# Kernel optimization log

Hardware: AMD Instinct MI355X
Metric: run time of the kernel (lower is better)

## Reference

```python
import jax, jax.numpy as jnp
import numpy as np

D_MODEL = 1024
HEADS = 16
HEAD_DIM = D_MODEL // HEADS


def setup_inputs() -> dict:
    key = jax.random.key(0)
    k_x, k_q, k_k, k_v, k_o = jax.random.split(key, 5)
    B, S = 4, 2048
    return {
        "x": jax.random.normal(k_x, (B, S, D_MODEL), dtype=jnp.float32),
        "W_q": jax.random.normal(k_q, (D_MODEL, D_MODEL), dtype=jnp.float32),
        "W_k": jax.random.normal(k_k, (D_MODEL, D_MODEL), dtype=jnp.float32),
        "W_v": jax.random.normal(k_v, (D_MODEL, D_MODEL), dtype=jnp.float32),
        "fc_out": jax.random.normal(k_o, (D_MODEL, D_MODEL), dtype=jnp.float32),
    }


def reference(x, W_q, W_k, W_v, fc_out):
    B, S, D = x.shape
    H, Hd = HEADS, HEAD_DIM
    # QKV projections (no bias)
    Q = jnp.matmul(x, W_q)  # [B,S,D]
    K = jnp.matmul(x, W_k)
    V = jnp.matmul(x, W_v)
    # split heads -> [B,H,S,Hd]
    Qh = Q.reshape(B, S, H, Hd).transpose(0, 2, 1, 3)
    Kh = K.reshape(B, S, H, Hd).transpose(0, 2, 1, 3)
    Vh = V.reshape(B, S, H, Hd).transpose(0, 2, 1, 3)
    # full unfused attention: materialize [B,H,S,S] scores, softmax over last dim
    scores = jnp.einsum("bhqd,bhkd->bhqk", Qh, Kh) / jnp.sqrt(jnp.float32(Hd))
    attn = jax.nn.softmax(scores, axis=-1)
    head_out = jnp.einsum("bhqk,bhkd->bhqd", attn, Vh)  # [B,H,S,Hd]
    merged = head_out.transpose(0, 2, 1, 3).reshape(B, S, D)
    return jnp.matmul(merged, fc_out)
```

## Files before the change

kernel.cpp:

```cpp
#include <hip/hip_runtime.h>
#include <stdint.h>

#define MROWS 8192
#define DM    1024
#define NH    16
#define HD    64
#define SEQ   2048

typedef __bf16 bf16x8 __attribute__((ext_vector_type(8)));
typedef __bf16 bf16x4 __attribute__((ext_vector_type(4)));
typedef float  floatx4 __attribute__((ext_vector_type(4)));

#define QSCALE 0.18033688011112042f

__device__ __forceinline__ void async16(const void* g, void* l) {
  __builtin_amdgcn_global_load_lds(
      (__attribute__((address_space(1))) void*)g,
      (__attribute__((address_space(3))) void*)l,
      16, 0, 0);
}

__device__ __forceinline__ floatx4 mfma16(bf16x8 a, bf16x8 b, floatx4 c) {
  return __builtin_amdgcn_mfma_f32_16x16x32_bf16(a, b, c, 0, 0, 0);
}


__global__ void __launch_bounds__(256) split_x_kernel(const float* __restrict__ x,
                                                      __bf16* __restrict__ xh,
                                                      __bf16* __restrict__ xl) {
  const int i = blockIdx.x * 256 + threadIdx.x;
  const float4 v = reinterpret_cast<const float4*>(x)[i];
  const float vv[4] = {v.x, v.y, v.z, v.w};
  bf16x4 H, L;
#pragma unroll
  for (int j = 0; j < 4; ++j) {
    const __bf16 h = (__bf16)vv[j];
    H[j] = h;
    L[j] = (__bf16)(vv[j] - (float)h);
  }
  reinterpret_cast<bf16x4*>(xh)[i] = H;
  reinterpret_cast<bf16x4*>(xl)[i] = L;
}

__global__ void __launch_bounds__(256) wtrans_kernel(const float* __restrict__ W,
                                                     __bf16* __restrict__ Th,
                                                     __bf16* __restrict__ Tl) {
  __shared__ float t[32][33];
  const int tx = threadIdx.x & 31, ty = threadIdx.x >> 5;
  const int bx = blockIdx.x & 31, by = blockIdx.x >> 5;
#pragma unroll
  for (int j = 0; j < 4; ++j) {
    const int k = by * 32 + ty + j * 8;
    t[ty + j * 8][tx] = W[(size_t)k * DM + bx * 32 + tx];
  }
  __syncthreads();
#pragma unroll
  for (int j = 0; j < 4; ++j) {
    const int n = bx * 32 + ty + j * 8;
    const int k = by * 32 + tx;
    const float v = t[tx][ty + j * 8];
    const __bf16 h = (__bf16)v;
    Th[(size_t)n * DM + k] = h;
    if (Tl) Tl[(size_t)n * DM + k] = (__bf16)(v - (float)h);
  }
}

template <int OUTMODE>
__global__ void __launch_bounds__(256) gemm_nt(const __bf16* __restrict__ Ah,
                                               const __bf16* __restrict__ Bh,
                                               void* __restrict__ C0) {
  __shared__ __align__(16) __bf16 sAh[128 * 32];
  __shared__ __align__(16) __bf16 sBh[128 * 32];

  const int tid = threadIdx.x;
  const int bm = blockIdx.x >> 3;
  const int bn = blockIdx.x & 7;
  const int m0 = bm << 7, n0 = bn << 7;
  const int w = tid >> 6;
  const int lane = tid & 63;
  const int wm = (w >> 1) << 6;
  const int wn = (w & 1) << 6;
  const int lm = lane & 15;
  const int q4 = lane >> 4;

  floatx4 acc[4][4];
  const floatx4 fz = {0.f, 0.f, 0.f, 0.f};
#pragma unroll
  for (int i = 0; i < 4; ++i)
#pragma unroll
    for (int j = 0; j < 4; ++j) acc[i][j] = fz;

  const int c0 = tid, c1 = tid + 256;
  const int row0 = c0 >> 2, cc0 = (c0 & 3) ^ ((row0 >> 1) & 3);
  const int row1 = c1 >> 2, cc1 = (c1 & 3) ^ ((row1 >> 1) & 3);

  int offA[4], offB[4];
#pragma unroll
  for (int i = 0; i < 4; ++i) {
    const int ra = wm + i * 16 + lm;
    offA[i] = ra * 32 + ((q4 ^ ((ra >> 1) & 3)) << 3);
    const int rb = wn + i * 16 + lm;
    offB[i] = rb * 32 + ((q4 ^ ((rb >> 1) & 3)) << 3);
  }

  size_t ga0 = (size_t)(m0 + row0) * DM + cc0 * 8;
  size_t gb0 = (size_t)(n0 + row0) * DM + cc0 * 8;
  size_t ga1 = (size_t)(m0 + row1) * DM + cc1 * 8;
  size_t gb1 = (size_t)(n0 + row1) * DM + cc1 * 8;

  for (int it = 0; it < 32; ++it) {
    async16(Ah + ga0, &sAh[c0 * 8]);
    async16(Bh + gb0, &sBh[c0 * 8]);
    async16(Ah + ga1, &sAh[c1 * 8]);
    async16(Bh + gb1, &sBh[c1 * 8]);
    ga0 += 32; gb0 += 32; ga1 += 32; gb1 += 32;
    __syncthreads();

    bf16x8 ah[4], bh[4];
#pragma unroll
    for (int i = 0; i < 4; ++i) {
      ah[i] = *(const bf16x8*)&sAh[offA[i]];
      bh[i] = *(const bf16x8*)&sBh[offB[i]];
    }
#pragma unroll
    for (int i = 0; i < 4; ++i)
#pragma unroll
      for (int j = 0; j < 4; ++j)
        acc[i][j] = mfma16(ah[i], bh[j], acc[i][j]);
    __syncthreads();
  }

#pragma unroll
  for (int i = 0; i < 4; ++i) {
#pragma unroll
    for (int j = 0; j < 4; ++j) {
#pragma unroll
      for (int r = 0; r < 4; ++r) {
        const int gr = m0 + wm + i * 16 + q4 * 4 + r;
        const int gc = n0 + wn + j * 16 + lm;
        const float v = acc[i][j][r];
        if constexpr (OUTMODE == 1) {
          ((float*)C0)[(size_t)gr * DM + gc] = v;
        } else {
          const int bb = gr >> 11, ss = gr & 2047;
          const int hh = gc >> 6, dd = gc & 63;
          ((__bf16*)C0)[(((size_t)(bb * NH + hh) << 6) + dd) * SEQ + ss] = (__bf16)v;
        }
      }
    }
  }
}

__global__ void __launch_bounds__(256, 2) gemm_qk(const __bf16* __restrict__ Ah,
                                                  const __bf16* __restrict__ Al,
                                                  const __bf16* __restrict__ Bqh,
                                                  const __bf16* __restrict__ Bql,
                                                  const __bf16* __restrict__ Bkh,
                                                  const __bf16* __restrict__ Bkl,
                                                  __bf16* __restrict__ Qh,
                                                  __bf16* __restrict__ Ql,
                                                  __bf16* __restrict__ Kh,
                                                  __bf16* __restrict__ Kl) {
  __shared__ __align__(16) __bf16 sAh[128 * 32];
  __shared__ __align__(16) __bf16 sAl[128 * 32];
  __shared__ __align__(16) __bf16 sQh_[128 * 32];
  __shared__ __align__(16) __bf16 sQl_[128 * 32];
  __shared__ __align__(16) __bf16 sKh_[128 * 32];
  __shared__ __align__(16) __bf16 sKl_[128 * 32];

  const int tid = threadIdx.x;
  const int bm = blockIdx.x >> 3;
  const int bn = blockIdx.x & 7;
  const int m0 = bm << 7, n0 = bn << 7;
  const int w = tid >> 6;
  const int lane = tid & 63;
  const int wm = (w >> 1) << 6;
  const int wn = (w & 1) << 6;
  const int lm = lane & 15;
  const int q4 = lane >> 4;

  floatx4 accq[4][4], acck[4][4];
  const floatx4 fz = {0.f, 0.f, 0.f, 0.f};
#pragma unroll
  for (int i = 0; i < 4; ++i)
#pragma unroll
    for (int j = 0; j < 4; ++j) { accq[i][j] = fz; acck[i][j] = fz; }

  const int c0 = tid, c1 = tid + 256;
  const int row0 = c0 >> 2, cc0 = (c0 & 3) ^ ((row0 >> 1) & 3);
  const int row1 = c1 >> 2, cc1 = (c1 & 3) ^ ((row1 >> 1) & 3);

  int offA[4], offB[4];
#pragma unroll
  for (int i = 0; i < 4; ++i) {
    const int ra = wm + i * 16 + lm;
    offA[i] = ra * 32 + ((q4 ^ ((ra >> 1) & 3)) << 3);
    const int rb = wn + i * 16 + lm;
    offB[i] = rb * 32 + ((q4 ^ ((rb >> 1) & 3)) << 3);
  }

  size_t ga0 = (size_t)(m0 + row0) * DM + cc0 * 8;
  size_t gb0 = (size_t)(n0 + row0) * DM + cc0 * 8;
  size_t ga1 = (size_t)(m0 + row1) * DM + cc1 * 8;
  size_t gb1 = (size_t)(n0 + row1) * DM + cc1 * 8;

  for (int it = 0; it < 32; ++it) {
    async16(Ah + ga0, &sAh[c0 * 8]);
    async16(Al + ga0, &sAl[c0 * 8]);
    async16(Ah + ga1, &sAh[c1 * 8]);
    async16(Al + ga1, &sAl[c1 * 8]);
    async16(Bqh + gb0, &sQh_[c0 * 8]);
    async16(Bql + gb0, &sQl_[c0 * 8]);
    async16(Bqh + gb1, &sQh_[c1 * 8]);
    async16(Bql + gb1, &sQl_[c1 * 8]);
    async16(Bkh + gb0, &sKh_[c0 * 8]);
    async16(Bkl + gb0, &sKl_[c0 * 8]);
    async16(Bkh + gb1, &sKh_[c1 * 8]);
    async16(Bkl + gb1, &sKl_[c1 * 8]);
    ga0 += 32; gb0 += 32; ga1 += 32; gb1 += 32;
    __syncthreads();

    bf16x8 ah[4], al[4];
#pragma unroll
    for (int i = 0; i < 4; ++i) {
      ah[i] = *(const bf16x8*)&sAh[offA[i]];
      al[i] = *(const bf16x8*)&sAl[offA[i]];
    }
    {
      bf16x8 bh[4], bl[4];
#pragma unroll
      for (int j = 0; j < 4; ++j) {
        bh[j] = *(const bf16x8*)&sQh_[offB[j]];
        bl[j] = *(const bf16x8*)&sQl_[offB[j]];
      }
#pragma unroll
      for (int i = 0; i < 4; ++i)
#pragma unroll
        for (int j = 0; j < 4; ++j) {
          accq[i][j] = mfma16(ah[i], bh[j], accq[i][j]);
          accq[i][j] = mfma16(ah[i], bl[j], accq[i][j]);
          accq[i][j] = mfma16(al[i], bh[j], accq[i][j]);
        }
    }
    {
      bf16x8 bh[4], bl[4];
#pragma unroll
      for (int j = 0; j < 4; ++j) {
        bh[j] = *(const bf16x8*)&sKh_[offB[j]];
        bl[j] = *(const bf16x8*)&sKl_[offB[j]];
      }
#pragma unroll
      for (int i = 0; i < 4; ++i)
#pragma unroll
        for (int j = 0; j < 4; ++j) {
          acck[i][j] = mfma16(ah[i], bh[j], acck[i][j]);
          acck[i][j] = mfma16(ah[i], bl[j], acck[i][j]);
          acck[i][j] = mfma16(al[i], bh[j], acck[i][j]);
        }
    }
    __syncthreads();
  }

#pragma unroll
  for (int i = 0; i < 4; ++i) {
#pragma unroll
    for (int j = 0; j < 4; ++j) {
#pragma unroll
      for (int r = 0; r < 4; ++r) {
        const int gr = m0 + wm + i * 16 + q4 * 4 + r;
        const int gc = n0 + wn + j * 16 + lm;
        const size_t idx = (size_t)gr * DM + gc;
        const float vq = accq[i][j][r] * QSCALE;
        const __bf16 qhv = (__bf16)vq;
        Qh[idx] = qhv;
        Ql[idx] = (__bf16)(vq - (float)qhv);
        const float vk = acck[i][j][r];
        const __bf16 khv = (__bf16)vk;
        Kh[idx] = khv;
        Kl[idx] = (__bf16)(vk - (float)khv);
      }
    }
  }
}

__global__ void __launch_bounds__(256, 3) flash_kernel(const __bf16* __restrict__ Qh,
                                                       const __bf16* __restrict__ Ql,
                                                       const __bf16* __restrict__ Kh,
                                                       const __bf16* __restrict__ Kl,
                                                       const __bf16* __restrict__ Vt,
                                                       __bf16* __restrict__ Mg) {
  __shared__ __align__(16) __bf16 sKh[64 * 64];
  __shared__ __align__(16) __bf16 sKl[64 * 64];
  __shared__ __align__(16) __bf16 sV[64 * 64];
  __shared__ __align__(16) __bf16 sP[4][32 * 72];

  const int tid = threadIdx.x;
  const int qt = blockIdx.x & 15;
  const int bh = blockIdx.x >> 4;
  const int b = bh >> 4;
  const int h = bh & 15;
  const int mq0 = b * SEQ + qt * 128;
  const int ch = h * 64;
  const int w = tid >> 6;
  const int lane = tid & 63;
  const int lm = lane & 15;
  const int q4 = lane >> 4;

  const int c0 = tid, c1 = tid + 256;
  const int r0 = c0 >> 3, e0 = ((c0 & 7) ^ (r0 & 7)) << 3;
  const int r1 = c1 >> 3, e1 = ((c1 & 7) ^ (r1 & 7)) << 3;

  bf16x8 qh[2][2], ql[2][2];
#pragma unroll
  for (int p = 0; p < 2; ++p) {
    const size_t gq0 = (size_t)(mq0 + p * 64 + r0) * DM + ch + e0;
    const size_t gq1 = (size_t)(mq0 + p * 64 + r1) * DM + ch + e1;
    async16(Qh + gq0, &sKh[c0 * 8]);
    async16(Ql + gq0, &sKl[c0 * 8]);
    async16(Qh + gq1, &sKh[c1 * 8]);
    async16(Ql + gq1, &sKl[c1 * 8]);
    __syncthreads();
    if ((w >> 1) == p) {
#pragma unroll
      for (int mi = 0; mi < 2; ++mi) {
        const int rq = (w & 1) * 32 + mi * 16 + lm;
#pragma unroll
        for (int ks = 0; ks < 2; ++ks) {
          const int oq = rq * 64 + (((ks * 4 + q4) ^ (rq & 7)) << 3);
          qh[mi][ks] = *(const bf16x8*)&sKh[oq];
          ql[mi][ks] = *(const bf16x8*)&sKl[oq];
        }
      }
    }
    __syncthreads();
  }

  int ofr[2][4];
#pragma unroll
  for (int ks = 0; ks < 2; ++ks)
#pragma unroll
    for (int t = 0; t < 4; ++t) {
      const int rk = t * 16 + lm;
      ofr[ks][t] = rk * 64 + (((ks * 4 + q4) ^ (rk & 7)) << 3);
    }

  floatx4 o[2][4];
  const floatx4 fz = {0.f, 0.f, 0.f, 0.f};
#pragma unroll
  for (int mi = 0; mi < 2; ++mi)
#pragma unroll
    for (int dt = 0; dt < 4; ++dt) o[mi][dt] = fz;
  float lsum[2] = {0.f, 0.f};
  float m[2] = {-1e30f, -1e30f};

  size_t gk0 = (size_t)(b * SEQ + r0) * DM + ch + e0;
  size_t gk1 = (size_t)(b * SEQ + r1) * DM + ch + e1;
  size_t gv0 = (size_t)(bh * 64 + r0) * SEQ + e0;
  size_t gv1 = (size_t)(bh * 64 + r1) * SEQ + e1;

  for (int it = 0; it < 32; ++it) {
    async16(Kh + gk0, &sKh[c0 * 8]);
    async16(Kl + gk0, &sKl[c0 * 8]);
    async16(Kh + gk1, &sKh[c1 * 8]);
    async16(Kl + gk1, &sKl[c1 * 8]);
    async16(Vt + gv0, &sV[c0 * 8]);
    async16(Vt + gv1, &sV[c1 * 8]);
    gk0 += (size_t)64 * DM;
    gk1 += (size_t)64 * DM;
    gv0 += 64;
    gv1 += 64;
    __syncthreads();

    floatx4 s2[4][2];
#pragma unroll
    for (int nt = 0; nt < 4; ++nt)
#pragma unroll
      for (int mi = 0; mi < 2; ++mi) s2[nt][mi] = fz;
#pragma unroll
    for (int ks = 0; ks < 2; ++ks) {
#pragma unroll
      for (int nt = 0; nt < 4; ++nt) {
        const bf16x8 kh = *(const bf16x8*)&sKh[ofr[ks][nt]];
        const bf16x8 kl = *(const bf16x8*)&sKl[ofr[ks][nt]];
#pragma unroll
        for (int mi = 0; mi < 2; ++mi) {
          s2[nt][mi] = mfma16(kh, qh[mi][ks], s2[nt][mi]);
          s2[nt][mi] = mfma16(kl, qh[mi][ks], s2[nt][mi]);
          s2[nt][mi] = mfma16(kh, ql[mi][ks], s2[nt][mi]);
        }
      }
    }

    float tm[2];
#pragma unroll
    for (int mi = 0; mi < 2; ++mi) {
      float mx = fmaxf(fmaxf(s2[0][mi][0], s2[0][mi][1]),
                       fmaxf(s2[0][mi][2], s2[0][mi][3]));
#pragma unroll
      for (int nt = 1; nt < 4; ++nt) {
        mx = fmaxf(mx, fmaxf(fmaxf(s2[nt][mi][0], s2[nt][mi][1]),
                             fmaxf(s2[nt][mi][2], s2[nt][mi][3])));
      }
      mx = fmaxf(mx, __shfl_xor(mx, 16));
      mx = fmaxf(mx, __shfl_xor(mx, 32));
      tm[mi] = mx;
    }
    if (__ballot((tm[0] > m[0] + 8.f) || (tm[1] > m[1] + 8.f))) {
#pragma unroll
      for (int mi = 0; mi < 2; ++mi) {
        const float mn = fmaxf(m[mi], tm[mi]);
        const float a = __builtin_amdgcn_exp2f(m[mi] - mn);
        m[mi] = mn;
        lsum[mi] *= a;
#pragma unroll
        for (int dt = 0; dt < 4; ++dt) o[mi][dt] *= a;
      }
    }

#pragma unroll
    for (int mi = 0; mi < 2; ++mi) {
      float ps = 0.f;
#pragma unroll
      for (int nt = 0; nt < 4; ++nt) {
        bf16x4 pk;
#pragma unroll
        for (int r = 0; r < 4; ++r) {
          const float p = __builtin_amdgcn_exp2f(s2[nt][mi][r] - m[mi]);
          ps += p;
          pk[r] = (__bf16)p;
        }
        *(bf16x4*)&sP[w][(mi * 16 + lm) * 72 + nt * 16 + q4 * 4] = pk;
      }
      ps += __shfl_xor(ps, 16);
      ps += __shfl_xor(ps, 32);
      lsum[mi] += ps;
    }

#pragma unroll
    for (int ks = 0; ks < 2; ++ks) {
      const bf16x8 a0 = *(const bf16x8*)&sP[w][lm * 72 + ks * 32 + q4 * 8];
      const bf16x8 a1 = *(const bf16x8*)&sP[w][(16 + lm) * 72 + ks * 32 + q4 * 8];
#pragma unroll
      for (int dt = 0; dt < 4; ++dt) {
        const bf16x8 bv = *(const bf16x8*)&sV[ofr[ks][dt]];
        o[0][dt] = mfma16(bv, a0, o[0][dt]);
        o[1][dt] = mfma16(bv, a1, o[1][dt]);
      }
    }
    __syncthreads();
  }

#pragma unroll
  for (int mi = 0; mi < 2; ++mi) {
    const float inv = __builtin_amdgcn_rcpf(lsum[mi]);
    const int gr = mq0 + w * 32 + mi * 16 + lm;
#pragma unroll
    for (int dt = 0; dt < 4; ++dt) {
      bf16x4 ov;
#pragma unroll
      for (int r = 0; r < 4; ++r) ov[r] = (__bf16)(o[mi][dt][r] * inv);
      *(bf16x4*)&Mg[(size_t)gr * DM + ch + dt * 16 + q4 * 4] = ov;
    }
  }
}


extern "C" void kernel_launch(void* const* d_in, const int* in_sizes, int n_in,
                              void* d_out, int out_size, void* d_ws, size_t ws_size,
                              hipStream_t stream) {
  (void)in_sizes; (void)n_in; (void)out_size; (void)ws_size;
  const float* x  = (const float*)d_in[0];
  const float* Wq = (const float*)d_in[1];
  const float* Wk = (const float*)d_in[2];
  const float* Wv = (const float*)d_in[3];
  const float* fc = (const float*)d_in[4];
  float* out = (float*)d_out;

  char* base = (char*)d_ws;
  const size_t XB = (size_t)MROWS * DM * 2;
  const size_t WB = (size_t)DM * DM * 2;
  __bf16* xh  = (__bf16*)(base);
  __bf16* xl  = (__bf16*)(base + XB);
  __bf16* wqh = (__bf16*)(base + 2 * XB);
  __bf16* wql = (__bf16*)(base + 2 * XB + WB);
  __bf16* wkh = (__bf16*)(base + 2 * XB + 2 * WB);
  __bf16* wkl = (__bf16*)(base + 2 * XB + 3 * WB);
  __bf16* wvh = (__bf16*)(base + 2 * XB + 4 * WB);
  __bf16* fch = (__bf16*)(base + 2 * XB + 5 * WB);
  __bf16* Qh  = (__bf16*)(base + 2 * XB + 6 * WB);
  __bf16* Ql  = (__bf16*)(base + 3 * XB + 6 * WB);
  __bf16* Kh  = (__bf16*)(base + 4 * XB + 6 * WB);
  __bf16* Kl  = (__bf16*)(base + 5 * XB + 6 * WB);
  __bf16* Vt  = xl;
  __bf16* Mg  = xh;

  split_x_kernel<<<dim3(8192), dim3(256), 0, stream>>>(x, xh, xl);
  wtrans_kernel<<<dim3(1024), dim3(256), 0, stream>>>(Wq, wqh, wql);
  wtrans_kernel<<<dim3(1024), dim3(256), 0, stream>>>(Wk, wkh, wkl);
  wtrans_kernel<<<dim3(1024), dim3(256), 0, stream>>>(Wv, wvh, (__bf16*)nullptr);
  wtrans_kernel<<<dim3(1024), dim3(256), 0, stream>>>(fc, fch, (__bf16*)nullptr);

  gemm_qk<<<dim3(512), dim3(256), 0, stream>>>(xh, xl, wqh, wql, wkh, wkl, Qh, Ql, Kh, Kl);
  gemm_nt<3><<<dim3(512), dim3(256), 0, stream>>>(xh, wvh, (void*)Vt);

  flash_kernel<<<dim3(1024), dim3(256), 0, stream>>>(Qh, Ql, Kh, Kl, Vt, Mg);

  gemm_nt<1><<<dim3(512), dim3(256), 0, stream>>>(Mg, fch, (void*)out);
}
```

Measured before the change: 408.0 us.

## Double-buffer K/V tiles in flash attention to overlap loads with compute

The flash attention kernel now keeps two shared-memory buffers for the K-high, K-low and V tiles. It prefetches the next tile while computing on the current one, and uses a single wait-plus-barrier per iteration instead of two __syncthreads. The aim is to hide global-to-LDS load latency behind the MFMA work. In exchange, LDS use roughly doubles and the occupancy hint drops from 3 to 2 blocks per SM, so there is less cross-block latency hiding.

```diff
diff --git a/kernel.cpp b/kernel.cpp
--- a/kernel.cpp
+++ b/kernel.cpp
@@ -283,15 +283,15 @@
   }
 }
 
-__global__ void __launch_bounds__(256, 3) flash_kernel(const __bf16* __restrict__ Qh,
+__global__ void __launch_bounds__(256, 2) flash_kernel(const __bf16* __restrict__ Qh,
                                                        const __bf16* __restrict__ Ql,
                                                        const __bf16* __restrict__ Kh,
                                                        const __bf16* __restrict__ Kl,
                                                        const __bf16* __restrict__ Vt,
                                                        __bf16* __restrict__ Mg) {
-  __shared__ __align__(16) __bf16 sKh[64 * 64];
-  __shared__ __align__(16) __bf16 sKl[64 * 64];
-  __shared__ __align__(16) __bf16 sV[64 * 64];
+  __shared__ __align__(16) __bf16 sKh[2][64 * 64];
+  __shared__ __align__(16) __bf16 sKl[2][64 * 64];
+  __shared__ __align__(16) __bf16 sV[2][64 * 64];
   __shared__ __align__(16) __bf16 sP[4][32 * 72];
 
   const int tid = threadIdx.x;
@@ -315,10 +315,10 @@
   for (int p = 0; p < 2; ++p) {
     const size_t gq0 = (size_t)(mq0 + p * 64 + r0) * DM + ch + e0;
     const size_t gq1 = (size_t)(mq0 + p * 64 + r1) * DM + ch + e1;
-    async16(Qh + gq0, &sKh[c0 * 8]);
-    async16(Ql + gq0, &sKl[c0 * 8]);
-    async16(Qh + gq1, &sKh[c1 * 8]);
-    async16(Ql + gq1, &sKl[c1 * 8]);
+    async16(Qh + gq0, &sKh[0][c0 * 8]);
+    async16(Ql + gq0, &sKl[0][c0 * 8]);
+    async16(Qh + gq1, &sKh[0][c1 * 8]);
+    async16(Ql + gq1, &sKl[0][c1 * 8]);
     __syncthreads();
     if ((w >> 1) == p) {
 #pragma unroll
@@ -327,8 +327,8 @@
 #pragma unroll
         for (int ks = 0; ks < 2; ++ks) {
           const int oq = rq * 64 + (((ks * 4 + q4) ^ (rq & 7)) << 3);
-          qh[mi][ks] = *(const bf16x8*)&sKh[oq];
-          ql[mi][ks] = *(const bf16x8*)&sKl[oq];
+          qh[mi][ks] = *(const bf16x8*)&sKh[0][oq];
+          ql[mi][ks] = *(const bf16x8*)&sKl[0][oq];
         }
       }
     }
@@ -358,18 +358,38 @@
   size_t gv0 = (size_t)(bh * 64 + r0) * SEQ + e0;
   size_t gv1 = (size_t)(bh * 64 + r1) * SEQ + e1;
 
+  async16(Kh + gk0, &sKh[0][c0 * 8]);
+  async16(Kl + gk0, &sKl[0][c0 * 8]);
+  async16(Kh + gk1, &sKh[0][c1 * 8]);
+  async16(Kl + gk1, &sKl[0][c1 * 8]);
+  async16(Vt + gv0, &sV[0][c0 * 8]);
+  async16(Vt + gv1, &sV[0][c1 * 8]);
+  gk0 += (size_t)64 * DM;
+  gk1 += (size_t)64 * DM;
+  gv0 += 64;
+  gv1 += 64;
+
   for (int it = 0; it < 32; ++it) {
-    async16(Kh + gk0, &sKh[c0 * 8]);
-    async16(Kl + gk0, &sKl[c0 * 8]);
-    async16(Kh + gk1, &sKh[c1 * 8]);
-    async16(Kl + gk1, &sKl[c1 * 8]);
-    async16(Vt + gv0, &sV[c0 * 8]);
-    async16(Vt + gv1, &sV[c1 * 8]);
-    gk0 += (size_t)64 * DM;
-    gk1 += (size_t)64 * DM;
-    gv0 += 64;
-    gv1 += 64;
-    __syncthreads();
+    const int cur = it & 1;
+    asm volatile("s_waitcnt vmcnt(0)" ::: "memory");
+    __builtin_amdgcn_s_barrier();
+    __builtin_amdgcn_sched_barrier(0);
+    if (it < 31) {
+      const int nxt = cur ^ 1;
+      async16(Kh + gk0, &sKh[nxt][c0 * 8]);
+      async16(Kl + gk0, &sKl[nxt][c0 * 8]);
+      async16(Kh + gk1, &sKh[nxt][c1 * 8]);
+      async16(Kl + gk1, &sKl[nxt][c1 * 8]);
+      async16(Vt + gv0, &sV[nxt][c0 * 8]);
+      async16(Vt + gv1, &sV[nxt][c1 * 8]);
+      gk0 += (size_t)64 * DM;
+      gk1 += (size_t)64 * DM;
+      gv0 += 64;
+      gv1 += 64;
+    }
+    const __bf16* bKh = sKh[cur];
+    const __bf16* bKl = sKl[cur];
+    const __bf16* bV = sV[cur];
 
     floatx4 s2[4][2];
 #pragma unroll
@@ -380,8 +400,8 @@
     for (int ks = 0; ks < 2; ++ks) {
 #pragma unroll
       for (int nt = 0; nt < 4; ++nt) {
-        const bf16x8 kh = *(const bf16x8*)&sKh[ofr[ks][nt]];
-        const bf16x8 kl = *(const bf16x8*)&sKl[ofr[ks][nt]];
+        const bf16x8 kh = *(const bf16x8*)&bKh[ofr[ks][nt]];
+        const bf16x8 kl = *(const bf16x8*)&bKl[ofr[ks][nt]];
 #pragma unroll
         for (int mi = 0; mi < 2; ++mi) {
           s2[nt][mi] = mfma16(kh, qh[mi][ks], s2[nt][mi]);
@@ -442,12 +462,11 @@
       const bf16x8 a1 = *(const bf16x8*)&sP[w][(16 + lm) * 72 + ks * 32 + q4 * 8];
 #pragma unroll
       for (int dt = 0; dt < 4; ++dt) {
-        const bf16x8 bv = *(const bf16x8*)&sV[ofr[ks][dt]];
+        const bf16x8 bv = *(const bf16x8*)&bV[ofr[ks][dt]];
         o[0][dt] = mfma16(bv, a0, o[0][dt]);
         o[1][dt] = mfma16(bv, a1, o[1][dt]);
       }
     }
-    __syncthreads();
   }
 
 #pragma unroll
```

After: 408.8 us. About the same (+0.2%).
